# Kernel optimization log

Hardware: AMD Instinct MI355X
Metric: run time of the kernel (lower is better)

The kernel has to match this reference:

```python
import jax, jax.numpy as jnp
import numpy as np

HEADS, LEVELS, POINTS, DIMS = 8, 4, 4, 256
CH = DIMS // HEADS
SHAPES = np.array([[96, 96], [48, 48], [24, 24], [12, 12]], dtype=np.int64)
LEVEL_START = np.concatenate([[0], np.cumsum(SHAPES[:, 0] * SHAPES[:, 1])[:-1]]).astype(np.int64)
HW = int((SHAPES[:, 0] * SHAPES[:, 1]).sum())
N, Q = 2, HW


def setup_inputs() -> dict:
    key = jax.random.key(0)
    ks = jax.random.split(key, 8)
    return {
        "q": jax.random.normal(ks[0], (N, Q, DIMS), jnp.float32),
        "p": jax.random.uniform(ks[1], (N, Q, LEVELS, 2), jnp.float32),
        "v": jax.random.normal(ks[2], (N, HW, DIMS), jnp.float32),
        "W_off": jax.random.normal(ks[3], (DIMS, HEADS * LEVELS * POINTS * 2), jnp.float32) * 0.01,
        "b_off": jax.random.normal(ks[4], (HEADS * LEVELS * POINTS * 2,), jnp.float32) * 0.5,
        "W_attn": jax.random.normal(ks[5], (DIMS, HEADS * LEVELS * POINTS), jnp.float32) * 0.02,
        "b_attn": jnp.zeros((HEADS * LEVELS * POINTS,), jnp.float32),
        "W_in": jax.random.normal(ks[6], (DIMS, DIMS), jnp.float32) / np.float32(np.sqrt(DIMS)),
        "b_in": jnp.zeros((DIMS,), jnp.float32),
        "W_out": jax.random.normal(ks[7], (DIMS, DIMS), jnp.float32) / np.float32(np.sqrt(DIMS)),
        "b_out": jnp.zeros((DIMS,), jnp.float32),
        "shapes": jnp.asarray(SHAPES),
        "level_index": jnp.asarray(LEVEL_START),
    }


def _sample_level(vl, loc_l, Hl, Wl):
    """Bilinear sample with zero padding outside the feature map.
    vl: [N, Hl*Wl, heads, C]; loc_l: [N, Q, heads, P, 2] normalized (x, y) in [0,1].
    Returns [N, Q, P, heads, C]."""
    Nb, Qn, Hd, P, _ = loc_l.shape
    x = loc_l[..., 0] * Wl - 0.5  # pixel coords, align_corners=False convention
    y = loc_l[..., 1] * Hl - 0.5
    x0 = jnp.floor(x)
    y0 = jnp.floor(y)
    dx = x - x0
    dy = y - y0
    x0i = x0.astype(jnp.int32)
    y0i = y0.astype(jnp.int32)
    out = jnp.zeros((Nb, Qn, P, Hd, vl.shape[-1]), vl.dtype)
    corners = ((x0i, y0i, (1 - dx) * (1 - dy)), (x0i + 1, y0i, dx * (1 - dy)),
               (x0i, y0i + 1, (1 - dx) * dy), (x0i + 1, y0i + 1, dx * dy))
    for cx, cy, w in corners:
        valid = (cx >= 0) & (cx < Wl) & (cy >= 0) & (cy < Hl)
        idx = jnp.clip(cy, 0, Hl - 1) * Wl + jnp.clip(cx, 0, Wl - 1)  # [N,Q,Hd,P]
        idx_t = idx.transpose(0, 1, 3, 2).reshape(Nb, Qn * P, Hd, 1)
        g = jnp.take_along_axis(vl, idx_t, axis=1).reshape(Nb, Qn, P, Hd, -1)
        wv = jnp.where(valid, w, 0.0).transpose(0, 1, 3, 2)  # [N,Q,P,Hd]
        out = out + g * wv[..., None].astype(vl.dtype)
    return out


def _forward(q, p, v, W_off, b_off, W_attn, b_attn, W_in, b_in, W_out, b_out, shp, lsi):
    Nb, Qn, _ = q.shape
    v = (v @ W_in + b_in).reshape(Nb, -1, HEADS, CH)
    off = (q @ W_off + b_off).reshape(Nb, Qn, HEADS, LEVELS, POINTS, 2)
    attn = jax.nn.softmax((q @ W_attn + b_attn).reshape(Nb, Qn, HEADS, LEVELS * POINTS), axis=-1)
    attn = attn.reshape(Nb, Qn, HEADS, LEVELS, POINTS)
    # offsets normalized by (W, H) of each level, added to reference points (2-coord branch)
    off_norm = jnp.asarray(np.stack([shp[:, 1], shp[:, 0]], -1), q.dtype)  # [L, 2]
    loc = p[:, :, None, :, None, :] + off / off_norm[None, None, None, :, None, :]  # [N,Q,Hd,L,P,2]
    out = jnp.zeros((Nb, Qn, HEADS, CH), q.dtype)
    for l in range(LEVELS):
        Hl, Wl = int(shp[l, 0]), int(shp[l, 1])
        s = int(lsi[l])
        vl = jax.lax.slice_in_dim(v, s, s + Hl * Wl, axis=1)
        samp = _sample_level(vl, loc[:, :, :, l], Hl, Wl)  # [N,Q,P,Hd,C]
        out = out + jnp.einsum('nqphc,nqhp->nqhc', samp, attn[:, :, :, l])
    return out.reshape(Nb, Qn, DIMS) @ W_out + b_out


def reference(q, p, v, W_off, b_off, W_attn, b_attn, W_in, b_in, W_out, b_out, shapes, level_index):
    shp = np.asarray(shapes)  # spatial shapes are structural constants
    lsi = np.asarray(level_index)
    return _forward(q, p, v, W_off, b_off, W_attn, b_attn, W_in, b_in, W_out, b_out, shp, lsi)
```

## Files before the change

### kernel.cpp

```cpp
#include <hip/hip_runtime.h>
#include <hip/hip_bf16.h>
#include <hip/hip_fp16.h>
#include <math.h>

#define NB      2
#define QN      12240
#define HW_TOT  12240
#define DIMS    256
#define HEADS   8
#define CH      32
#define LEVELS  4
#define POINTS  4
#define M_TOT   (NB * QN)

typedef unsigned short ushort_t;
typedef __attribute__((ext_vector_type(8))) short short8;
typedef __attribute__((ext_vector_type(4))) float floatx4;

__device__ __forceinline__ ushort_t f2bf(float f) {
    __hip_bfloat16 h = __float2bfloat16(f);
    return *reinterpret_cast<ushort_t*>(&h);
}
__device__ __forceinline__ ushort_t f2h(float f) {
    __half h = __float2half(f);
    return *reinterpret_cast<ushort_t*>(&h);
}

__global__ __launch_bounds__(256) void prep_weights_kernel(
    const float* __restrict__ W_in, const float* __restrict__ W_off,
    const float* __restrict__ W_attn, const float* __restrict__ W_out,
    const float* __restrict__ b_off, const float* __restrict__ b_attn,
    ushort_t* __restrict__ Tin, ushort_t* __restrict__ Tcomb,
    ushort_t* __restrict__ Tout, float* __restrict__ bcomb,
    int* __restrict__ vpad)
{
    const int gi = blockIdx.x * 256 + threadIdx.x;
    if (gi < 32)  vpad[gi] = 0;
    if (gi < 384) bcomb[gi] = (gi < 256) ? b_off[gi] : b_attn[gi - 256];
    const int k = gi & 255;
    const int n = gi >> 8;
    if (gi < 65536) {
        Tin[n * 256 + k]  = f2bf(W_in[k * 256 + n]);
        Tout[n * 256 + k] = f2bf(W_out[k * 256 + n]);
    }
    const float val = (n < 256) ? W_off[k * 256 + n]
                                : W_attn[k * 128 + (n - 256)];
    Tcomb[n * 256 + k] = f2bf(val);
}

template<int CMODE, bool DUAL>
__device__ __forceinline__ void gemm_fused_tile(
    const float* __restrict__ A32, const ushort_t* __restrict__ BT,
    const float* __restrict__ bias, void* __restrict__ C,
    int M, int Nc, int bm0, int bn0a, int bn0b,
    ushort_t* As, ushort_t* Bs0, ushort_t* Bs1)
{
    const int tid  = threadIdx.x;
    const int wave = tid >> 6;
    const int lane = tid & 63;
    const int quad = lane >> 4;
    const int l16  = lane & 15;
    const int wm   = (wave >> 1) * 64;
    const int wn   = (wave & 1) * 64;

    const int off0 = tid * 16;
    const int row0 = off0 >> 6;
    const int kc0  = (off0 & 63) >> 1;

    int ar0 = bm0 + row0;      if (ar0 > M - 1) ar0 = M - 1;
    int ar1 = bm0 + row0 + 64; if (ar1 > M - 1) ar1 = M - 1;

    const float*    gA0  = A32 + (size_t)ar0 * 256 + kc0;
    const float*    gA1  = A32 + (size_t)ar1 * 256 + kc0;
    const ushort_t* gb0a = BT + (size_t)(bn0a + row0) * 256 + kc0;
    const ushort_t* gb1a = BT + (size_t)(bn0a + row0 + 64) * 256 + kc0;
    const ushort_t* gb0b = BT + (size_t)(bn0b + row0) * 256 + kc0;
    const ushort_t* gb1b = BT + (size_t)(bn0b + row0 + 64) * 256 + kc0;

    ushort_t* lB0a = Bs0 + wave * 512;
    ushort_t* lB1a = Bs0 + wave * 512 + 2048;
    ushort_t* lB0b = Bs1 + wave * 512;
    ushort_t* lB1b = Bs1 + wave * 512 + 2048;

    floatx4 acc0[4][4], acc1[4][4];
    #pragma unroll
    for (int i = 0; i < 4; ++i)
        #pragma unroll
        for (int j = 0; j < 4; ++j) {
            acc0[i][j] = (floatx4){0.f, 0.f, 0.f, 0.f};
            if (DUAL) acc1[i][j] = (floatx4){0.f, 0.f, 0.f, 0.f};
        }

    for (int kk = 0; kk < 256; kk += 32) {
        __builtin_amdgcn_global_load_lds(
            (const __attribute__((address_space(1))) void*)(gb0a + kk),
            (__attribute__((address_space(3))) void*)lB0a, 16, 0, 0);
        __builtin_amdgcn_global_load_lds(
            (const __attribute__((address_space(1))) void*)(gb1a + kk),
            (__attribute__((address_space(3))) void*)lB1a, 16, 0, 0);
        if (DUAL) {
            __builtin_amdgcn_global_load_lds(
                (const __attribute__((address_space(1))) void*)(gb0b + kk),
                (__attribute__((address_space(3))) void*)lB0b, 16, 0, 0);
            __builtin_amdgcn_global_load_lds(
                (const __attribute__((address_space(1))) void*)(gb1b + kk),
                (__attribute__((address_space(3))) void*)lB1b, 16, 0, 0);
        }
        {
            const float4 a0 = *(const float4*)(gA0 + kk);
            const float4 a1 = *(const float4*)(gA0 + kk + 4);
            const float4 b0 = *(const float4*)(gA1 + kk);
            const float4 b1 = *(const float4*)(gA1 + kk + 4);
            ushort_t t0[8] = {f2bf(a0.x), f2bf(a0.y), f2bf(a0.z), f2bf(a0.w),
                              f2bf(a1.x), f2bf(a1.y), f2bf(a1.z), f2bf(a1.w)};
            ushort_t t1[8] = {f2bf(b0.x), f2bf(b0.y), f2bf(b0.z), f2bf(b0.w),
                              f2bf(b1.x), f2bf(b1.y), f2bf(b1.z), f2bf(b1.w)};
            *(int4*)&As[tid * 8]        = *(int4*)t0;
            *(int4*)&As[tid * 8 + 2048] = *(int4*)t1;
        }
        __syncthreads();

        short8 af[4], bfa[4], bfb[4];
        #pragma unroll
        for (int mt = 0; mt < 4; ++mt)
            af[mt] = *(const short8*)&As[(wm + mt * 16 + l16) * 32 + quad * 8];
        #pragma unroll
        for (int nt = 0; nt < 4; ++nt) {
            bfa[nt] = *(const short8*)&Bs0[(wn + nt * 16 + l16) * 32 + quad * 8];
            if (DUAL)
                bfb[nt] = *(const short8*)&Bs1[(wn + nt * 16 + l16) * 32 + quad * 8];
        }
        #pragma unroll
        for (int mt = 0; mt < 4; ++mt)
            #pragma unroll
            for (int nt = 0; nt < 4; ++nt) {
                acc0[mt][nt] = __builtin_amdgcn_mfma_f32_16x16x32_bf16(
                    af[mt], bfa[nt], acc0[mt][nt], 0, 0, 0);
                if (DUAL)
                    acc1[mt][nt] = __builtin_amdgcn_mfma_f32_16x16x32_bf16(
                        af[mt], bfb[nt], acc1[mt][nt], 0, 0, 0);
            }
        __syncthreads();
    }

    #pragma unroll
    for (int mt = 0; mt < 4; ++mt) {
        #pragma unroll
        for (int j = 0; j < 4; ++j) {
            const int row = bm0 + wm + mt * 16 + quad * 4 + j;
            if (row >= M) continue;
            #pragma unroll
            for (int nt = 0; nt < 4; ++nt) {
                {
                    const int col = bn0a + wn + nt * 16 + l16;
                    const float val = acc0[mt][nt][j] + bias[col];
                    if (CMODE == 1) {
                        const size_t idx = (((size_t)(col >> 5) * M + row) << 5) + (col & 31);
                        ((ushort_t*)C)[idx] = f2bf(val);
                    } else {
                        ((ushort_t*)C)[(size_t)row * Nc + col] = f2h(val);
                    }
                }
                if (DUAL) {
                    const int col = bn0b + wn + nt * 16 + l16;
                    const float val = acc1[mt][nt][j] + bias[col];
                    if (CMODE == 1) {
                        const size_t idx = (((size_t)(col >> 5) * M + row) << 5) + (col & 31);
                        ((ushort_t*)C)[idx] = f2bf(val);
                    } else {
                        ((ushort_t*)C)[(size_t)row * Nc + col] = f2h(val);
                    }
                }
            }
        }
    }
}

__global__ __launch_bounds__(256) void gemm_proj_kernel(
    const float* __restrict__ v, const float* __restrict__ q,
    const ushort_t* __restrict__ Tin, const ushort_t* __restrict__ Tcomb,
    const float* __restrict__ b_in, const float* __restrict__ bcomb,
    ushort_t* __restrict__ vproj, ushort_t* __restrict__ offh)
{
    __shared__ ushort_t As [128 * 32];
    __shared__ ushort_t Bs0[128 * 32];
    __shared__ ushort_t Bs1[128 * 32];
    const int bm0 = blockIdx.x * 128;
    const int y = blockIdx.y;
    if (y == 0)
        gemm_fused_tile<1, true >(v, Tin,   b_in,  vproj, M_TOT, 256, bm0, 0, 128, As, Bs0, Bs1);
    else if (y == 1)
        gemm_fused_tile<2, true >(q, Tcomb, bcomb, offh,  M_TOT, 384, bm0, 0, 128, As, Bs0, Bs1);
    else
        gemm_fused_tile<2, false>(q, Tcomb, bcomb, offh,  M_TOT, 384, bm0, 256, 0, As, Bs0, Bs1);
}

__device__ __forceinline__ void gemm_tile_core(
    const ushort_t* __restrict__ A, const ushort_t* __restrict__ BT,
    const float* __restrict__ bias, float* __restrict__ C,
    int M, int Nc, int bm0, int bn0, int K,
    ushort_t* As, ushort_t* Bs)
{
    const int tid  = threadIdx.x;
    const int wave = tid >> 6;
    const int lane = tid & 63;
    const int quad = lane >> 4;
    const int l16  = lane & 15;
    const int wm   = (wave >> 1) * 64;
    const int wn   = (wave & 1) * 64;

    const int off0 = tid * 16;
    const int row0 = off0 >> 6;
    const int kc0  = (off0 & 63) >> 1;

    int ar0 = bm0 + row0;      if (ar0 > M - 1) ar0 = M - 1;
    int ar1 = bm0 + row0 + 64; if (ar1 > M - 1) ar1 = M - 1;

    const ushort_t* ga0 = A  + (size_t)ar0 * K + kc0;
    const ushort_t* ga1 = A  + (size_t)ar1 * K + kc0;
    const ushort_t* gb0 = BT + (size_t)(bn0 + row0) * K + kc0;
    const ushort_t* gb1 = BT + (size_t)(bn0 + row0 + 64) * K + kc0;

    ushort_t* lA0 = As + wave * 512;
    ushort_t* lA1 = As + wave * 512 + 2048;
    ushort_t* lB0 = Bs + wave * 512;
    ushort_t* lB1 = Bs + wave * 512 + 2048;

    floatx4 acc[4][4];
    #pragma unroll
    for (int i = 0; i < 4; ++i)
        #pragma unroll
        for (int j = 0; j < 4; ++j)
            acc[i][j] = (floatx4){0.f, 0.f, 0.f, 0.f};

    for (int kk = 0; kk < K; kk += 32) {
        __builtin_amdgcn_global_load_lds(
            (const __attribute__((address_space(1))) void*)(ga0 + kk),
            (__attribute__((address_space(3))) void*)lA0, 16, 0, 0);
        __builtin_amdgcn_global_load_lds(
            (const __attribute__((address_space(1))) void*)(ga1 + kk),
            (__attribute__((address_space(3))) void*)lA1, 16, 0, 0);
        __builtin_amdgcn_global_load_lds(
            (const __attribute__((address_space(1))) void*)(gb0 + kk),
            (__attribute__((address_space(3))) void*)lB0, 16, 0, 0);
        __builtin_amdgcn_global_load_lds(
            (const __attribute__((address_space(1))) void*)(gb1 + kk),
            (__attribute__((address_space(3))) void*)lB1, 16, 0, 0);
        __syncthreads();

        short8 af[4], bfr[4];
        #pragma unroll
        for (int mt = 0; mt < 4; ++mt)
            af[mt] = *(const short8*)&As[(wm + mt * 16 + l16) * 32 + quad * 8];
        #pragma unroll
        for (int nt = 0; nt < 4; ++nt)
            bfr[nt] = *(const short8*)&Bs[(wn + nt * 16 + l16) * 32 + quad * 8];
        #pragma unroll
        for (int mt = 0; mt < 4; ++mt)
            #pragma unroll
            for (int nt = 0; nt < 4; ++nt)
                acc[mt][nt] = __builtin_amdgcn_mfma_f32_16x16x32_bf16(
                    af[mt], bfr[nt], acc[mt][nt], 0, 0, 0);
        __syncthreads();
    }

    #pragma unroll
    for (int mt = 0; mt < 4; ++mt) {
        #pragma unroll
        for (int j = 0; j < 4; ++j) {
            const int row = bm0 + wm + mt * 16 + quad * 4 + j;
            if (row >= M) continue;
            #pragma unroll
            for (int nt = 0; nt < 4; ++nt) {
                const int col = bn0 + wn + nt * 16 + l16;
                C[(size_t)row * Nc + col] = acc[mt][nt][j] + bias[col];
            }
        }
    }
}

__global__ __launch_bounds__(256) void gemm_out_kernel(
    const ushort_t* __restrict__ mid, const ushort_t* __restrict__ Tout,
    const float* __restrict__ b_out, float* __restrict__ out)
{
    __shared__ ushort_t As[128 * 32];
    __shared__ ushort_t Bs[128 * 32];
    gemm_tile_core(mid, Tout, b_out, out, M_TOT, 256,
                   blockIdx.x * 128, blockIdx.y * 128, 256, As, Bs);
}

#define LO32(u) __uint_as_float((u) << 16)
#define HI32(u) __uint_as_float((u) & 0xffff0000u)
#define ACC8(W, g) \
    a0 = fmaf(W, LO32(g.x), a0);  a1 = fmaf(W, HI32(g.x), a1); \
    a2 = fmaf(W, LO32(g.y), a2);  a3 = fmaf(W, HI32(g.y), a3); \
    a4 = fmaf(W, LO32(g.z), a4);  a5 = fmaf(W, HI32(g.z), a5); \
    a6 = fmaf(W, LO32(g.w), a6);  a7 = fmaf(W, HI32(g.w), a7);

__global__ __launch_bounds__(256, 8) void msda_sample_kernel(
    const ushort_t* __restrict__ vproj, const ushort_t* __restrict__ offh,
    const float* __restrict__ p, ushort_t* __restrict__ mid)
{
    __shared__ int4 s_main[4][68];
    __shared__ int2 s_aux[4][68];

    const int tid = threadIdx.x;
    const int wv  = tid >> 6;
    const int l   = tid & 63;
    const int idx = blockIdx.x;
    const int b8  = idx & 7;
    const int hh  = b8 >> 2;
    const int qg  = (idx >> 3) * 4 + (b8 & 3);
    const int nq  = qg * 4 + wv;
    const int nb  = (nq >= QN) ? 1 : 0;

    const size_t orow = (size_t)nq * 384;
    const __half2 o2 = *(const __half2*)&offh[orow + hh * 128 + 2 * l];
    const float2  of = __half22float2(o2);
    const float   lg = __half2float(
        *(const __half*)&offh[orow + 256 + hh * 64 + l]);
    const int     lvl = (l >> 2) & 3;
    const float2  pl  = *(const float2*)&p[(size_t)nq * 8 + lvl * 2];

    float mx = lg;
    #pragma unroll
    for (int m = 8; m; m >>= 1) mx = fmaxf(mx, __shfl_xor(mx, m));
    const float e = __expf(lg - mx);
    float ss = e;
    #pragma unroll
    for (int m = 8; m; m >>= 1) ss += __shfl_xor(ss, m);
    const float wt = e * __builtin_amdgcn_rcpf(ss);

    const int   Wl = 96 >> lvl;
    const float fW = (float)Wl;
    const int   st = 12288 - (12288 >> (2 * lvl));
    const int   h4 = l >> 4;
    const int   h  = hh * 4 + h4;

    {
        const float x  = fmaf(pl.x, fW, of.x) - 0.5f;
        const float y  = fmaf(pl.y, fW, of.y) - 0.5f;
        const float xf = floorf(x), yf = floorf(y);
        const float dx = x - xf,    dy = y - yf;
        const int   x0 = (int)xf,   y0 = (int)yf;
        const bool vxl = (unsigned)x0       < (unsigned)Wl;
        const bool vxr = (unsigned)(x0 + 1) < (unsigned)Wl;
        const bool vy0 = (unsigned)y0       < (unsigned)Wl;
        const bool vy1 = (unsigned)(y0 + 1) < (unsigned)Wl;

        const float wxl = vxl ? (1.0f - dx) : (vxr ? dx : 0.0f);
        const float wxr = (vxl && vxr) ? dx : 0.0f;
        const int   xb  = vxl ? x0 : 0;

        const float wy0f = wt * (1.0f - dy), wy1f = wt * dy;
        const float w_l0 = vy0 ? wxl * wy0f : 0.0f;
        const float w_r0 = vy0 ? wxr * wy0f : 0.0f;
        const float w_l1 = vy1 ? wxl * wy1f : 0.0f;
        const float w_r1 = vy1 ? wxr * wy1f : 0.0f;

        int yc0 = y0;     if (yc0 < 0) yc0 = 0; if (yc0 > Wl - 1) yc0 = Wl - 1;
        int yc1 = y0 + 1; if (yc1 < 0) yc1 = 0; if (yc1 > Wl - 1) yc1 = Wl - 1;

        const int rowb = h * M_TOT + nb * HW_TOT + st + xb;
        const int lin0 = rowb + yc0 * Wl;
        const int lin1 = rowb + yc1 * Wl;
        const int e17 = h4 * 17 + (l & 15);
        s_main[wv][e17] = (int4){lin0 << 6, __float_as_int(w_l0),
                                 __float_as_int(w_r0), lin1 << 6};
        s_aux[wv][e17]  = (int2){__float_as_int(w_l1), __float_as_int(w_r1)};
    }

    __builtin_amdgcn_wave_barrier();
    asm volatile("s_waitcnt lgkmcnt(0)" ::: "memory");
    __builtin_amdgcn_wave_barrier();

    const int hg     = l >> 4;
    const int rowr   = (l >> 3) & 1;
    const int corner = (l >> 2) & 1;
    const int c16    = (l & 7) * 16;
    const char* __restrict__ vb = (const char*)vproj;

    float a0 = 0.f, a1 = 0.f, a2 = 0.f, a3 = 0.f;
    float a4 = 0.f, a5 = 0.f, a6 = 0.f, a7 = 0.f;

    #pragma unroll 4
    for (int t = 0; t < 16; ++t) {
        const int  e17 = hg * 17 + t;
        const int4 c   = s_main[wv][e17];
        const int2 cb  = s_aux[wv][e17];
        const int  base = rowr ? c.w : c.x;
        const float wl  = rowr ? __int_as_float(cb.x) : __int_as_float(c.y);
        const float wr  = rowr ? __int_as_float(cb.y) : __int_as_float(c.z);
        const float w   = corner ? wr : wl;
        const uint4 g   = *(const uint4*)(vb + (unsigned)(base + c16));
        ACC8(w, g);
    }

    a0 += __shfl_xor(a0, 4);  a1 += __shfl_xor(a1, 4);
    a2 += __shfl_xor(a2, 4);  a3 += __shfl_xor(a3, 4);
    a4 += __shfl_xor(a4, 4);  a5 += __shfl_xor(a5, 4);
    a6 += __shfl_xor(a6, 4);  a7 += __shfl_xor(a7, 4);
    a0 += __shfl_xor(a0, 8);  a1 += __shfl_xor(a1, 8);
    a2 += __shfl_xor(a2, 8);  a3 += __shfl_xor(a3, 8);
    a4 += __shfl_xor(a4, 8);  a5 += __shfl_xor(a5, 8);
    a6 += __shfl_xor(a6, 8);  a7 += __shfl_xor(a7, 8);

    if ((l & 12) == 0) {
        ushort_t mv[8] = {f2bf(a0), f2bf(a1), f2bf(a2), f2bf(a3),
                          f2bf(a4), f2bf(a5), f2bf(a6), f2bf(a7)};
        const int col = (hh * 4 + hg) * 32 + (l & 3) * 8;
        *(uint4*)&mid[(size_t)nq * 256 + col] = *(uint4*)mv;
    }
}

extern "C" void kernel_launch(void* const* d_in, const int* in_sizes, int n_in,
                              void* d_out, int out_size, void* d_ws, size_t ws_size,
                              hipStream_t stream)
{
    const float* q      = (const float*)d_in[0];
    const float* p      = (const float*)d_in[1];
    const float* v      = (const float*)d_in[2];
    const float* W_off  = (const float*)d_in[3];
    const float* b_off  = (const float*)d_in[4];
    const float* W_attn = (const float*)d_in[5];
    const float* b_attn = (const float*)d_in[6];
    const float* W_in   = (const float*)d_in[7];
    const float* b_in   = (const float*)d_in[8];
    const float* W_out  = (const float*)d_in[9];
    const float* b_out  = (const float*)d_in[10];
    float* out = (float*)d_out;

    const int M = M_TOT;

    ushort_t* vproj  = (ushort_t*)d_ws;
    ushort_t* vpad   = vproj + (size_t)M * 256;
    ushort_t* offh   = vpad + 64;
    ushort_t* mid    = offh + (size_t)M * 384;
    ushort_t* Tin    = mid + (size_t)M * 256;
    ushort_t* Tcomb  = Tin + 256 * 256;
    ushort_t* Tout   = Tcomb + 384 * 256;
    float*    bcomb  = (float*)(Tout + 256 * 256);

    prep_weights_kernel<<<dim3(384), 256, 0, stream>>>(
        W_in, W_off, W_attn, W_out, b_off, b_attn,
        Tin, Tcomb, Tout, bcomb, (int*)vpad);

    gemm_proj_kernel<<<dim3(192, 3), 256, 0, stream>>>(
        v, q, Tin, Tcomb, b_in, bcomb, vproj, offh);
    msda_sample_kernel<<<dim3(12240), 256, 0, stream>>>(vproj, offh, p, mid);
    gemm_out_kernel<<<dim3(192, 2), 256, 0, stream>>>(mid, Tout, b_out, out);
}
```

Measured before the change: 178.1 us.

## Double-buffer LDS tiles in projection and output GEMMs to overlap loads with MFMA

Both GEMM tile routines now use two LDS buffers per operand. The next K-slice is prefetched via global_load_lds and register loads while MFMAs run on the current slice, and the fp32-to-bf16 conversion of A is deferred until after the compute. This hides global memory latency and drops one barrier per K step. In exchange LDS use per block doubles, which can lower occupancy. gemm_tile_core's loop is now hardcoded to 8 steps, so it assumes K equals 256.

```diff
diff --git a/kernel.cpp b/kernel.cpp
--- a/kernel.cpp
+++ b/kernel.cpp
@@ -26,6 +26,10 @@
     return *reinterpret_cast<ushort_t*>(&h);
 }
 
+#define GLOAD16(gp, lp) __builtin_amdgcn_global_load_lds( \
+    (const __attribute__((address_space(1))) void*)(gp),  \
+    (__attribute__((address_space(3))) void*)(lp), 16, 0, 0)
+
 __global__ __launch_bounds__(256) void prep_weights_kernel(
     const float* __restrict__ W_in, const float* __restrict__ W_off,
     const float* __restrict__ W_attn, const float* __restrict__ W_out,
@@ -53,7 +57,7 @@
     const float* __restrict__ A32, const ushort_t* __restrict__ BT,
     const float* __restrict__ bias, void* __restrict__ C,
     int M, int Nc, int bm0, int bn0a, int bn0b,
-    ushort_t* As, ushort_t* Bs0, ushort_t* Bs1)
+    ushort_t* AsB, ushort_t* Bs0B, ushort_t* Bs1B)
 {
     const int tid  = threadIdx.x;
     const int wave = tid >> 6;
@@ -77,11 +81,6 @@
     const ushort_t* gb0b = BT + (size_t)(bn0b + row0) * 256 + kc0;
     const ushort_t* gb1b = BT + (size_t)(bn0b + row0 + 64) * 256 + kc0;
 
-    ushort_t* lB0a = Bs0 + wave * 512;
-    ushort_t* lB1a = Bs0 + wave * 512 + 2048;
-    ushort_t* lB0b = Bs1 + wave * 512;
-    ushort_t* lB1b = Bs1 + wave * 512 + 2048;
-
     floatx4 acc0[4][4], acc1[4][4];
     #pragma unroll
     for (int i = 0; i < 4; ++i)
@@ -91,35 +90,46 @@
             if (DUAL) acc1[i][j] = (floatx4){0.f, 0.f, 0.f, 0.f};
         }
 
-    for (int kk = 0; kk < 256; kk += 32) {
-        __builtin_amdgcn_global_load_lds(
-            (const __attribute__((address_space(1))) void*)(gb0a + kk),
-            (__attribute__((address_space(3))) void*)lB0a, 16, 0, 0);
-        __builtin_amdgcn_global_load_lds(
-            (const __attribute__((address_space(1))) void*)(gb1a + kk),
-            (__attribute__((address_space(3))) void*)lB1a, 16, 0, 0);
+    float4 arg[4];
+
+    {
+        ushort_t* l0 = Bs0B + wave * 512;
+        GLOAD16(gb0a, l0); GLOAD16(gb1a, l0 + 2048);
         if (DUAL) {
-            __builtin_amdgcn_global_load_lds(
-                (const __attribute__((address_space(1))) void*)(gb0b + kk),
-                (__attribute__((address_space(3))) void*)lB0b, 16, 0, 0);
-            __builtin_amdgcn_global_load_lds(
-                (const __attribute__((address_space(1))) void*)(gb1b + kk),
-                (__attribute__((address_space(3))) void*)lB1b, 16, 0, 0);
-        }
-        {
-            const float4 a0 = *(const float4*)(gA0 + kk);
-            const float4 a1 = *(const float4*)(gA0 + kk + 4);
-            const float4 b0 = *(const float4*)(gA1 + kk);
-            const float4 b1 = *(const float4*)(gA1 + kk + 4);
-            ushort_t t0[8] = {f2bf(a0.x), f2bf(a0.y), f2bf(a0.z), f2bf(a0.w),
-                              f2bf(a1.x), f2bf(a1.y), f2bf(a1.z), f2bf(a1.w)};
-            ushort_t t1[8] = {f2bf(b0.x), f2bf(b0.y), f2bf(b0.z), f2bf(b0.w),
-                              f2bf(b1.x), f2bf(b1.y), f2bf(b1.z), f2bf(b1.w)};
-            *(int4*)&As[tid * 8]        = *(int4*)t0;
-            *(int4*)&As[tid * 8 + 2048] = *(int4*)t1;
-        }
-        __syncthreads();
-
+            ushort_t* l1 = Bs1B + wave * 512;
+            GLOAD16(gb0b, l1); GLOAD16(gb1b, l1 + 2048);
+        }
+        arg[0] = *(const float4*)(gA0);     arg[1] = *(const float4*)(gA0 + 4);
+        arg[2] = *(const float4*)(gA1);     arg[3] = *(const float4*)(gA1 + 4);
+        ushort_t t0[8] = {f2bf(arg[0].x), f2bf(arg[0].y), f2bf(arg[0].z), f2bf(arg[0].w),
+                          f2bf(arg[1].x), f2bf(arg[1].y), f2bf(arg[1].z), f2bf(arg[1].w)};
+        ushort_t t1[8] = {f2bf(arg[2].x), f2bf(arg[2].y), f2bf(arg[2].z), f2bf(arg[2].w),
+                          f2bf(arg[3].x), f2bf(arg[3].y), f2bf(arg[3].z), f2bf(arg[3].w)};
+        *(int4*)&AsB[tid * 8]        = *(int4*)t0;
+        *(int4*)&AsB[tid * 8 + 2048] = *(int4*)t1;
+    }
+    __syncthreads();
+
+    #pragma unroll
+    for (int t = 0; t < 8; ++t) {
+        const int cur = t & 1;
+        const int kkn = (t + 1) * 32;
+        if (t < 7) {
+            ushort_t* l0 = Bs0B + (cur ^ 1) * 4096 + wave * 512;
+            GLOAD16(gb0a + kkn, l0); GLOAD16(gb1a + kkn, l0 + 2048);
+            if (DUAL) {
+                ushort_t* l1 = Bs1B + (cur ^ 1) * 4096 + wave * 512;
+                GLOAD16(gb0b + kkn, l1); GLOAD16(gb1b + kkn, l1 + 2048);
+            }
+            arg[0] = *(const float4*)(gA0 + kkn);
+            arg[1] = *(const float4*)(gA0 + kkn + 4);
+            arg[2] = *(const float4*)(gA1 + kkn);
+            arg[3] = *(const float4*)(gA1 + kkn + 4);
+        }
+
+        const ushort_t* As  = AsB  + cur * 4096;
+        const ushort_t* Bs0 = Bs0B + cur * 4096;
+        const ushort_t* Bs1 = Bs1B + cur * 4096;
         short8 af[4], bfa[4], bfb[4];
         #pragma unroll
         for (int mt = 0; mt < 4; ++mt)
@@ -140,6 +150,16 @@
                     acc1[mt][nt] = __builtin_amdgcn_mfma_f32_16x16x32_bf16(
                         af[mt], bfb[nt], acc1[mt][nt], 0, 0, 0);
             }
+
+        if (t < 7) {
+            ushort_t t0[8] = {f2bf(arg[0].x), f2bf(arg[0].y), f2bf(arg[0].z), f2bf(arg[0].w),
+                              f2bf(arg[1].x), f2bf(arg[1].y), f2bf(arg[1].z), f2bf(arg[1].w)};
+            ushort_t t1[8] = {f2bf(arg[2].x), f2bf(arg[2].y), f2bf(arg[2].z), f2bf(arg[2].w),
+                              f2bf(arg[3].x), f2bf(arg[3].y), f2bf(arg[3].z), f2bf(arg[3].w)};
+            ushort_t* Asn = AsB + (cur ^ 1) * 4096;
+            *(int4*)&Asn[tid * 8]        = *(int4*)t0;
+            *(int4*)&Asn[tid * 8 + 2048] = *(int4*)t1;
+        }
         __syncthreads();
     }
 
@@ -182,9 +202,9 @@
     const float* __restrict__ b_in, const float* __restrict__ bcomb,
     ushort_t* __restrict__ vproj, ushort_t* __restrict__ offh)
 {
-    __shared__ ushort_t As [128 * 32];
-    __shared__ ushort_t Bs0[128 * 32];
-    __shared__ ushort_t Bs1[128 * 32];
+    __shared__ ushort_t As [2 * 128 * 32];
+    __shared__ ushort_t Bs0[2 * 128 * 32];
+    __shared__ ushort_t Bs1[2 * 128 * 32];
     const int bm0 = blockIdx.x * 128;
     const int y = blockIdx.y;
     if (y == 0)
@@ -199,7 +219,7 @@
     const ushort_t* __restrict__ A, const ushort_t* __restrict__ BT,
     const float* __restrict__ bias, float* __restrict__ C,
     int M, int Nc, int bm0, int bn0, int K,
-    ushort_t* As, ushort_t* Bs)
+    ushort_t* AsB, ushort_t* BsB)
 {
     const int tid  = threadIdx.x;
     const int wave = tid >> 6;
@@ -221,11 +241,6 @@
     const ushort_t* gb0 = BT + (size_t)(bn0 + row0) * K + kc0;
     const ushort_t* gb1 = BT + (size_t)(bn0 + row0 + 64) * K + kc0;
 
-    ushort_t* lA0 = As + wave * 512;
-    ushort_t* lA1 = As + wave * 512 + 2048;
-    ushort_t* lB0 = Bs + wave * 512;
-    ushort_t* lB1 = Bs + wave * 512 + 2048;
-
     floatx4 acc[4][4];
     #pragma unroll
     for (int i = 0; i < 4; ++i)
@@ -233,21 +248,27 @@
         for (int j = 0; j < 4; ++j)
             acc[i][j] = (floatx4){0.f, 0.f, 0.f, 0.f};
 
-    for (int kk = 0; kk < K; kk += 32) {
-        __builtin_amdgcn_global_load_lds(
-            (const __attribute__((address_space(1))) void*)(ga0 + kk),
-            (__attribute__((address_space(3))) void*)lA0, 16, 0, 0);
-        __builtin_amdgcn_global_load_lds(
-            (const __attribute__((address_space(1))) void*)(ga1 + kk),
-            (__attribute__((address_space(3))) void*)lA1, 16, 0, 0);
-        __builtin_amdgcn_global_load_lds(
-            (const __attribute__((address_space(1))) void*)(gb0 + kk),
-            (__attribute__((address_space(3))) void*)lB0, 16, 0, 0);
-        __builtin_amdgcn_global_load_lds(
-            (const __attribute__((address_space(1))) void*)(gb1 + kk),
-            (__attribute__((address_space(3))) void*)lB1, 16, 0, 0);
-        __syncthreads();
-
+    {
+        ushort_t* lA = AsB + wave * 512;
+        ushort_t* lB = BsB + wave * 512;
+        GLOAD16(ga0, lA); GLOAD16(ga1, lA + 2048);
+        GLOAD16(gb0, lB); GLOAD16(gb1, lB + 2048);
+    }
+    __syncthreads();
+
+    #pragma unroll
+    for (int t = 0; t < 8; ++t) {
+        const int cur = t & 1;
+        const int kkn = (t + 1) * 32;
+        if (t < 7) {
+            ushort_t* lA = AsB + (cur ^ 1) * 4096 + wave * 512;
+            ushort_t* lB = BsB + (cur ^ 1) * 4096 + wave * 512;
+            GLOAD16(ga0 + kkn, lA); GLOAD16(ga1 + kkn, lA + 2048);
+            GLOAD16(gb0 + kkn, lB); GLOAD16(gb1 + kkn, lB + 2048);
+        }
+
+        const ushort_t* As = AsB + cur * 4096;
+        const ushort_t* Bs = BsB + cur * 4096;
         short8 af[4], bfr[4];
         #pragma unroll
         for (int mt = 0; mt < 4; ++mt)
@@ -283,8 +304,8 @@
     const ushort_t* __restrict__ mid, const ushort_t* __restrict__ Tout,
     const float* __restrict__ b_out, float* __restrict__ out)
 {
-    __shared__ ushort_t As[128 * 32];
-    __shared__ ushort_t Bs[128 * 32];
+    __shared__ ushort_t As[2 * 128 * 32];
+    __shared__ ushort_t Bs[2 * 128 * 32];
     gemm_tile_core(mid, Tout, b_out, out, M_TOT, 256,
                    blockIdx.x * 128, blockIdx.y * 128, 256, As, Bs);
 }
```

New measurement: 183.3 us. 2.9% more time.
